# Optimization experiments

Hardware: AMD Instinct MI355X
Metric: run time of the kernel (lower is better)

Reference implementation:

```python
import jax, jax.numpy as jnp
import numpy as np

K = 10          # number of neighbors (init kwarg k)
NUM_CLASSES = 100  # label vocabulary (targets drawn in [0, 100))


def setup_inputs() -> dict:
    key = jax.random.key(0)
    k1, k2, k3 = jax.random.split(key, 3)
    X = jax.random.normal(k1, (1024, 512), dtype=jnp.float32)
    data = jax.random.normal(k2, (50000, 512), dtype=jnp.float32)
    targets = jax.random.randint(k3, (50000,), 0, NUM_CLASSES, dtype=jnp.int64)
    return {"X": X, "data": data, "targets": targets}


def reference(X, data, targets):
    # Pairwise L2 distance (p=2 path of the module), computed via the
    x2 = jnp.sum(X * X, axis=1, keepdims=True)              # [Q, 1]
    d2 = jnp.sum(data * data, axis=1)                        # [N]
    sq = x2 + d2[None, :] - 2.0 * (X @ data.T)               # [Q, N]
    dist = jnp.sqrt(jnp.maximum(sq, 0.0))                    # torch.norm(p1-p2, p=2)

    # torch: sort distances ascending, take first k indices -> top-k smallest.
    _, idx = jax.lax.top_k(-dist, K)                         # [Q, K]
    labels = targets[idx]                                    # [Q, K]

    # torch.mode over the k neighbor labels: histogram + argmax.
    # argmax picks the first (smallest) class on ties, matching torch.mode.
    counts = jax.nn.one_hot(labels, NUM_CLASSES, dtype=jnp.float32).sum(axis=1)  # [Q, C]
    pred = jnp.argmax(counts, axis=1).astype(jnp.float32)    # [Q]
    return pred
```

## Files before the change

### kernel.cpp

```cpp
#include <hip/hip_runtime.h>
#include <math.h>
#include <limits.h>

#define QN 1024
#define NN 50000
#define NPAD 50048
#define DD 512
#define KNN 10
#define NT 128
#define QTB 128
#define BK 32
#define NS 391
#define QB 8
#define NSAMP 63
#define NREST (NS - NSAMP)
#define CAP 512
#define SLACK 4.0f
#define LCAP 1152

#define WS_D2  0
#define WS_TAU 50048
#define WS_CNT (WS_TAU + 1024)
#define WS_XH  (WS_CNT + 1024)
#define WS_CKS (WS_XH + QN * DD / 2)
#define WS_BUF (WS_CKS + QN * NSAMP * KNN * 2)
#define WS_DH  (WS_BUF + QN * CAP * 2)
#define WS_END (WS_DH + NS * 16 * 2048)

typedef __attribute__((ext_vector_type(8))) short short8;
typedef __attribute__((ext_vector_type(4))) float f32x4;
typedef unsigned long long u64;

__device__ __forceinline__ u64 mkkey(float f, int idx) {
  unsigned u = __float_as_uint(f);
  unsigned m = u ^ ((unsigned)((int)u >> 31) | 0x80000000u);
  return ((u64)m << 32) | (unsigned)idx;
}

__device__ __forceinline__ float keyhi_f(unsigned m) {
  unsigned u = (m & 0x80000000u) ? (m ^ 0x80000000u) : ~m;
  return __uint_as_float(u);
}

__device__ __forceinline__ unsigned cvth(float x, float y) {
  unsigned ux = __float_as_uint(x), uy = __float_as_uint(y);
  unsigned rx = ux + 0x7fffu + ((ux >> 16) & 1u);
  unsigned ry = uy + 0x7fffu + ((uy >> 16) & 1u);
  return (rx >> 16) | (ry & 0xffff0000u);
}

__device__ __forceinline__ void glds16(const void* g, void* l) {
  __builtin_amdgcn_global_load_lds(
      (const __attribute__((address_space(1))) unsigned*)g,
      (__attribute__((address_space(3))) unsigned*)l, 16, 0, 0);
}

__device__ __forceinline__ void ins10(u64* kl, u64 k) {
#pragma unroll
  for (int u = 0; u < KNN; u++) {
    u64 lo = (k < kl[u]) ? k : kl[u];
    u64 hi = (k < kl[u]) ? kl[u] : k;
    kl[u] = lo; k = hi;
  }
}

__global__ __launch_bounds__(256) void conv_kernel(
    const float* __restrict__ dat, const float* __restrict__ Xm,
    float* __restrict__ ws) {
  if ((int)blockIdx.x >= NS) {
    const int g = ((int)blockIdx.x - NS) * 256 + threadIdx.x;
    const int b = g >> 10, kc = (g >> 6) & 15, l = g & 63;
    const int row = b * 16 + (l & 15);
    const int col = kc * 32 + (l >> 4) * 8;
    const float4* p = (const float4*)(Xm + (size_t)row * DD + col);
    float4 v0 = p[0], v1 = p[1];
    ((uint4*)(ws + WS_XH))[g] = make_uint4(
        cvth(v0.x, v0.y), cvth(v0.z, v0.w), cvth(v1.x, v1.y), cvth(v1.z, v1.w));
    return;
  }
  const int slice = blockIdx.x;
  const int t = threadIdx.x;
  const int row = t >> 1, h2 = t & 1;
  const int gr = slice * NT + row;
  const int r15 = row & 15;
  float s = 0.f;
#pragma unroll
  for (int kc8 = 0; kc8 < 8; kc8++) {
    const int kc = h2 * 8 + kc8;
    float4 v[8];
    if (gr < NN) {
      const float4* src = (const float4*)(dat + (size_t)gr * DD + kc * 32);
#pragma unroll
      for (int j = 0; j < 8; j++) v[j] = src[j];
    } else {
#pragma unroll
      for (int j = 0; j < 8; j++) v[j] = make_float4(0.f, 0.f, 0.f, 0.f);
    }
    unsigned hw[16];
#pragma unroll
    for (int j = 0; j < 8; j++) {
      s = fmaf(v[j].x, v[j].x, s); s = fmaf(v[j].y, v[j].y, s);
      s = fmaf(v[j].z, v[j].z, s); s = fmaf(v[j].w, v[j].w, s);
      hw[2 * j]     = cvth(v[j].x, v[j].y);
      hw[2 * j + 1] = cvth(v[j].z, v[j].w);
    }
    uint4* dhp = (uint4*)((unsigned char*)(ws + WS_DH) +
                          (((size_t)slice * 16 + kc) * 8 + (row >> 4)) * 1024);
#pragma unroll
    for (int qd = 0; qd < 4; qd++)
      dhp[qd * 16 + r15] = make_uint4(hw[4 * qd], hw[4 * qd + 1], hw[4 * qd + 2], hw[4 * qd + 3]);
  }
  s += __shfl_xor(s, 1, 64);
  if (h2 == 0) ws[WS_D2 + gr] = (gr < NN) ? s : __builtin_inff();
}

struct StageT { unsigned char bh[8192]; };
struct EpiT  { float sq[64][132]; };
struct ListT { u64 kl[64][4][KNN]; };

template <int MODE> struct SmemSel {
  union U { StageT s; EpiT e; ListT l; };
};
template <> struct SmemSel<1> {
  struct U { StageT s; float tau[128]; };
};

template <int PRE, int MODE>
__global__ __launch_bounds__(256, 3) void knn_chunk(
    const float* __restrict__ dat, float* __restrict__ ws, int soff) {
  __shared__ __align__(16) typename SmemSel<MODE>::U sm;
  int bqx, bsy;
  if (MODE == 1 && (gridDim.y & 7) == 0) {
    const int n = (int)(blockIdx.y * gridDim.x + blockIdx.x);
    const int m = n >> 3;
    const int ypx = (int)(gridDim.y >> 3);
    bqx = m & 7;
    bsy = (n & 7) * ypx + (m >> 3);
  } else {
    bqx = blockIdx.x; bsy = blockIdx.y;
  }
  const int qbase = bqx * QTB;
  const int slice = bsy + soff;
  const int nbase = slice * NT;
  const int t = threadIdx.x;
  const int lane = t & 63, wave = t >> 6;
  const int wn = wave & 1, wq = wave >> 1;
  const unsigned char* dh = (const unsigned char*)(ws + WS_DH);
  const char* xfh = (const char*)(ws + WS_XH);
  const int abase = (((bqx * 8 + wq * 4) * 16) * 64 + lane) * 16;

  f32x4 acc[4][4];
#pragma unroll
  for (int i = 0; i < 4; i++)
#pragma unroll
    for (int j = 0; j < 4; j++) acc[i][j] = (f32x4)0.f;

  auto stageB = [&](int kc) {
#pragma unroll
    for (int i = 0; i < 2; i++) {
      int p = wave * 2 + i;
      const unsigned char* g = dh +
          (((size_t)slice * 16 + kc) * 8 + p) * 1024 + lane * 16;
      glds16(g, sm.s.bh + p * 1024);
    }
  };

  if (PRE) {
    stageB(0);
    for (int kc = 0; kc < 16; kc++) {
      short8 fah[4];
#pragma unroll
      for (int i = 0; i < 4; i++)
        fah[i] = *(const short8*)(xfh + abase + i * 16384 + kc * 1024);
      __syncthreads();
      const int fragoff = lane * 16;
      short8 fbh[4];
#pragma unroll
      for (int i = 0; i < 4; i++)
        fbh[i] = *(const short8*)(sm.s.bh + (wn * 4 + i) * 1024 + fragoff);
      __syncthreads();
      if (kc < 15) stageB(kc + 1);
#pragma unroll
      for (int mt = 0; mt < 4; mt++)
#pragma unroll
        for (int nt = 0; nt < 4; nt++)
          acc[mt][nt] = __builtin_amdgcn_mfma_f32_16x16x32_bf16(fah[mt], fbh[nt], acc[mt][nt], 0, 0, 0);
    }
  } else {
    const int brow = t >> 1, bh_half = t & 1;
    const int bgr = nbase + brow;
    const int bpanel = (brow >> 4) * 1024;
    const int bchunk = (brow & 15) * 16;
    for (int kc = 0; kc < 16; kc++) {
      const int kk = kc * BK;
      short8 fah[4];
#pragma unroll
      for (int i = 0; i < 4; i++)
        fah[i] = *(const short8*)(xfh + abase + i * 16384 + kc * 1024);
      __syncthreads();
      {
        float4 v0 = make_float4(0.f, 0.f, 0.f, 0.f), v1 = v0, v2 = v0, v3 = v0;
        if (bgr < NN) {
          const float4* src = (const float4*)(dat + (size_t)bgr * DD + kk + bh_half * 16);
          v0 = src[0]; v1 = src[1]; v2 = src[2]; v3 = src[3];
        }
        unsigned char* bhp = sm.s.bh + bpanel;
        *(uint4*)(bhp + (2 * bh_half) * 256 + bchunk) =
            make_uint4(cvth(v0.x, v0.y), cvth(v0.z, v0.w), cvth(v1.x, v1.y), cvth(v1.z, v1.w));
        *(uint4*)(bhp + (2 * bh_half + 1) * 256 + bchunk) =
            make_uint4(cvth(v2.x, v2.y), cvth(v2.z, v2.w), cvth(v3.x, v3.y), cvth(v3.z, v3.w));
      }
      __syncthreads();
      const int fragoff = lane * 16;
      short8 fbh[4];
#pragma unroll
      for (int i = 0; i < 4; i++)
        fbh[i] = *(const short8*)(sm.s.bh + (wn * 4 + i) * 1024 + fragoff);
      __syncthreads();
#pragma unroll
      for (int mt = 0; mt < 4; mt++)
#pragma unroll
        for (int nt = 0; nt < 4; nt++)
          acc[mt][nt] = __builtin_amdgcn_mfma_f32_16x16x32_bf16(fah[mt], fbh[nt], acc[mt][nt], 0, 0, 0);
    }
  }

  if constexpr (MODE == 0) {
#pragma unroll
    for (int pass = 0; pass < 2; pass++) {
      __syncthreads();
      if (wq == pass) {
#pragma unroll
        for (int nt = 0; nt < 4; nt++) {
          int col = wn * 64 + nt * 16 + (lane & 15);
          float d2v = ws[WS_D2 + nbase + col];
#pragma unroll
          for (int mt = 0; mt < 4; mt++)
#pragma unroll
            for (int rg = 0; rg < 4; rg++) {
              int lr = mt * 16 + (lane >> 4) * 4 + rg;
              sm.e.sq[lr][col] = fmaf(-2.f, acc[mt][nt][rg], d2v);
            }
        }
      }
      __syncthreads();
      {
        const int r = t >> 2, s = t & 3;
        u64 kl[KNN];
#pragma unroll
        for (int u = 0; u < KNN; u++) kl[u] = ~0ull;
        for (int jj = 0; jj < 32; jj++) {
          int c = s * 32 + ((jj + r + 8 * s) & 31);
          float v = sm.e.sq[r][c];
          ins10(kl, mkkey(v, nbase + c));
        }
        __syncthreads();
#pragma unroll
        for (int u = 0; u < KNN; u++) sm.l.kl[r][s][u] = kl[u];
      }
      __syncthreads();
      if (t < 64) {
        u64* dst = ((u64*)(ws + WS_CKS)) +
                   ((size_t)(qbase + pass * 64 + t) * NSAMP + blockIdx.y) * KNN;
        int h0 = 0, h1 = 0, h2 = 0, h3 = 0;
        for (int pick = 0; pick < KNN; pick++) {
          u64 k0 = sm.l.kl[t][0][h0], k1 = sm.l.kl[t][1][h1];
          u64 k2 = sm.l.kl[t][2][h2], k3 = sm.l.kl[t][3][h3];
          u64 best = k0; int bm = 0;
          if (k1 < best) { best = k1; bm = 1; }
          if (k2 < best) { best = k2; bm = 2; }
          if (k3 < best) { best = k3; bm = 3; }
          dst[pick] = best;
          h0 += (bm == 0); h1 += (bm == 1); h2 += (bm == 2); h3 += (bm == 3);
        }
      }
    }
  } else {
    if (t < 128) sm.tau[t] = ws[WS_TAU + qbase + t];
    __syncthreads();
    unsigned* cnt = (unsigned*)(ws + WS_CNT);
    u64* buf = (u64*)(ws + WS_BUF);
    float d2v[4];
#pragma unroll
    for (int nt = 0; nt < 4; nt++)
      d2v[nt] = ws[WS_D2 + nbase + wn * 64 + nt * 16 + (lane & 15)];
#pragma unroll
    for (int mt = 0; mt < 4; mt++)
#pragma unroll
      for (int rg = 0; rg < 4; rg++) {
        int row = wq * 64 + mt * 16 + (lane >> 4) * 4 + rg;
        float tr = sm.tau[row];
#pragma unroll
        for (int nt = 0; nt < 4; nt++) {
          float d = fmaf(-2.f, acc[mt][nt][rg], d2v[nt]);
          if (d < tr) {
            int col = nbase + wn * 64 + nt * 16 + (lane & 15);
            int q = qbase + row;
            unsigned slot = atomicAdd(cnt + q, 1u);
            if (slot < CAP) buf[(size_t)q * CAP + slot] = mkkey(d, col);
          }
        }
      }
  }
}

__global__ __launch_bounds__(64) void tau_kernel(float* __restrict__ ws) {
  const int q = blockIdx.x;
  const int t = threadIdx.x;
  const u64* samp = ((const u64*)(ws + WS_CKS)) + (size_t)q * NSAMP * KNN;
  const int NC = NSAMP * KNN;
  u64 kl[KNN];
#pragma unroll
  for (int u = 0; u < KNN; u++) kl[u] = ~0ull;
  for (int j = t; j < NC; j += 64) ins10(kl, samp[j]);
  __shared__ u64 wk[64][KNN];
  __shared__ u64 m2[8][KNN];
#pragma unroll
  for (int u = 0; u < KNN; u++) wk[t][u] = kl[u];
  __syncthreads();
  if (t < 8) {
    int h[8] = {0, 0, 0, 0, 0, 0, 0, 0};
    for (int pick = 0; pick < KNN; pick++) {
      u64 best = ~0ull; int bm = 0;
#pragma unroll
      for (int m = 0; m < 8; m++) {
        u64 km = wk[t * 8 + m][h[m]];
        if (km < best) { best = km; bm = m; }
      }
      m2[t][pick] = best;
#pragma unroll
      for (int m = 0; m < 8; m++) h[m] += (bm == m);
    }
  }
  __syncthreads();
  if (t == 0) {
    int h[8] = {0, 0, 0, 0, 0, 0, 0, 0};
    u64 best = 0;
    for (int pick = 0; pick < KNN; pick++) {
      best = ~0ull; int bm = 0;
#pragma unroll
      for (int m = 0; m < 8; m++) {
        u64 km = m2[m][h[m]];
        if (km < best) { best = km; bm = m; }
      }
#pragma unroll
      for (int m = 0; m < 8; m++) h[m] += (bm == m);
    }
    ws[WS_TAU + q] = keyhi_f((unsigned)(best >> 32)) + SLACK;
    ((unsigned*)(ws + WS_CNT))[q] = 0u;
  }
}

__global__ __launch_bounds__(256) void knn_final(
    const int* __restrict__ targets, const float* __restrict__ Xm,
    const float* __restrict__ dat, float* __restrict__ ws,
    float* __restrict__ out) {
  const int q = blockIdx.x;
  const int t = threadIdx.x;
  const int lane = t & 63, wave = t >> 6;
  __shared__ float qrow[DD];
  __shared__ unsigned lst[LCAP];
  __shared__ int nlist;
  __shared__ u64 wk4[4][KNN];
  if (t == 0) nlist = 0;
  if (t < 128) ((float4*)qrow)[t] = ((const float4*)(Xm + (size_t)q * DD))[t];
  __syncthreads();
  const float tr = ws[WS_TAU + q];
  const u64* samp = ((const u64*)(ws + WS_CKS)) + (size_t)q * NSAMP * KNN;
  for (int j = t; j < NSAMP * KNN; j += 256) {
    u64 k = samp[j];
    if (keyhi_f((unsigned)(k >> 32)) < tr) {
      int s_ = atomicAdd(&nlist, 1);
      if (s_ < LCAP) lst[s_] = (unsigned)k;
    }
  }
  unsigned c = ((const unsigned*)(ws + WS_CNT))[q];
  if (c > CAP) c = CAP;
  const u64* buf = ((const u64*)(ws + WS_BUF)) + (size_t)q * CAP;
  for (int j = t; j < (int)c; j += 256) {
    int s_ = atomicAdd(&nlist, 1);
    if (s_ < LCAP) lst[s_] = (unsigned)buf[j];
  }
  __syncthreads();
  const int n = nlist < LCAP ? nlist : LCAP;

  u64 kl[KNN];
#pragma unroll
  for (int u = 0; u < KNN; u++) kl[u] = ~0ull;
  const float4* qv = (const float4*)qrow;
  const float4 q0 = qv[lane * 2], q1 = qv[lane * 2 + 1];
  for (int j = wave; j < n; j += 4) {
    const unsigned idx = lst[j];
    const float4* xr = (const float4*)(dat + (size_t)idx * DD) + lane * 2;
    const float4 a0 = xr[0], a1 = xr[1];
    float p = a0.x * q0.x;
    p = fmaf(a0.y, q0.y, p); p = fmaf(a0.z, q0.z, p); p = fmaf(a0.w, q0.w, p);
    p = fmaf(a1.x, q1.x, p); p = fmaf(a1.y, q1.y, p);
    p = fmaf(a1.z, q1.z, p); p = fmaf(a1.w, q1.w, p);
#pragma unroll
    for (int s_ = 1; s_ < 64; s_ <<= 1) p += __shfl_xor(p, s_, 64);
    float d = fmaf(-2.f, p, ws[WS_D2 + idx]);
    ins10(kl, mkkey(d, (int)idx));
  }
  if (lane == 0)
#pragma unroll
    for (int u = 0; u < KNN; u++) wk4[wave][u] = kl[u];
  __syncthreads();
  if (t == 0) {
    int h[4] = {0, 0, 0, 0};
    int fi[KNN];
    for (int pick = 0; pick < KNN; pick++) {
      u64 best = ~0ull; int bm = 0;
#pragma unroll
      for (int m = 0; m < 4; m++) {
        u64 km = wk4[m][h[m]];
        if (km < best) { best = km; bm = m; }
      }
      fi[pick] = (int)(unsigned)(best & 0xffffffffu);
      h[bm]++;
    }
    int lab[KNN];
#pragma unroll
    for (int u = 0; u < KNN; u++) lab[u] = targets[fi[u]];
    int bc = 0, bl = INT_MAX;
#pragma unroll
    for (int i = 0; i < KNN; i++) {
      int cc = 0;
#pragma unroll
      for (int j = 0; j < KNN; j++) cc += (lab[j] == lab[i]) ? 1 : 0;
      if (cc > bc || (cc == bc && lab[i] < bl)) { bc = cc; bl = lab[i]; }
    }
    out[q] = (float)bl;
  }
}

extern "C" void kernel_launch(void* const* d_in, const int* in_sizes, int n_in,
                              void* d_out, int out_size, void* d_ws, size_t ws_size,
                              hipStream_t stream) {
  const float* Xm  = (const float*)d_in[0];
  const float* dat = (const float*)d_in[1];
  const int* targets = (const int*)d_in[2];
  float* out = (float*)d_out;
  float* ws  = (float*)d_ws;
  const bool pre = ws_size >= (size_t)WS_END * 4;

  hipLaunchKernelGGL(conv_kernel, dim3(NS + QN * DD / 8 / 256), dim3(256), 0,
                     stream, dat, Xm, ws);
  if (pre) {
    hipLaunchKernelGGL((knn_chunk<1, 0>), dim3(QB, NSAMP), dim3(256), 0, stream, dat, ws, 0);
    hipLaunchKernelGGL(tau_kernel, dim3(QN), dim3(64), 0, stream, ws);
    hipLaunchKernelGGL((knn_chunk<1, 1>), dim3(QB, NREST), dim3(256), 0, stream, dat, ws, NSAMP);
  } else {
    hipLaunchKernelGGL((knn_chunk<0, 0>), dim3(QB, NSAMP), dim3(256), 0, stream, dat, ws, 0);
    hipLaunchKernelGGL(tau_kernel, dim3(QN), dim3(64), 0, stream, ws);
    hipLaunchKernelGGL((knn_chunk<0, 1>), dim3(QB, NREST), dim3(256), 0, stream, dat, ws, NSAMP);
  }
  hipLaunchKernelGGL(knn_final, dim3(QN), dim3(256), 0, stream, targets, Xm, dat, ws, out);
}
```

Baseline: 317.5 us.

## Halve sample slices, register-prefetch GEMM fragments, and unroll the exact rerank loop

Reduces the number of sampled slices used to estimate the per-query threshold from 63 to 31, shrinking the first-pass work. The precomputed-B GEMM path drops the global-to-LDS staging and its barriers, loading A and B fragments straight into registers with one-step software prefetch. The exact rerank loop processes two candidates per wave iteration and skips the insertion when a key cannot enter the top-10. A looser threshold from fewer samples may admit more candidates and overflow the buffer caps, and the register-only path raises register pressure and loses LDS sharing of B across waves.

```diff
diff --git a/kernel.cpp b/kernel.cpp
--- a/kernel.cpp
+++ b/kernel.cpp
@@ -12,7 +12,7 @@
 #define BK 32
 #define NS 391
 #define QB 8
-#define NSAMP 63
+#define NSAMP 31
 #define NREST (NS - NSAMP)
 #define CAP 512
 #define SLACK 4.0f
@@ -47,12 +47,6 @@
   unsigned rx = ux + 0x7fffu + ((ux >> 16) & 1u);
   unsigned ry = uy + 0x7fffu + ((uy >> 16) & 1u);
   return (rx >> 16) | (ry & 0xffff0000u);
-}
-
-__device__ __forceinline__ void glds16(const void* g, void* l) {
-  __builtin_amdgcn_global_load_lds(
-      (const __attribute__((address_space(1))) unsigned*)g,
-      (__attribute__((address_space(3))) unsigned*)l, 16, 0, 0);
 }
 
 __device__ __forceinline__ void ins10(u64* kl, u64 k) {
@@ -118,17 +112,16 @@
 struct EpiT  { float sq[64][132]; };
 struct ListT { u64 kl[64][4][KNN]; };
 
-template <int MODE> struct SmemSel {
-  union U { StageT s; EpiT e; ListT l; };
-};
-template <> struct SmemSel<1> {
-  struct U { StageT s; float tau[128]; };
-};
+template <int PRE, int MODE> struct Smem;
+template <> struct Smem<1, 0> { union { EpiT e; ListT l; }; };
+template <> struct Smem<1, 1> { float tau[128]; };
+template <> struct Smem<0, 0> { union { StageT s; EpiT e; ListT l; }; };
+template <> struct Smem<0, 1> { StageT s; float tau[128]; };
 
 template <int PRE, int MODE>
 __global__ __launch_bounds__(256, 3) void knn_chunk(
     const float* __restrict__ dat, float* __restrict__ ws, int soff) {
-  __shared__ __align__(16) typename SmemSel<MODE>::U sm;
+  __shared__ __align__(16) Smem<PRE, MODE> sm;
   int bqx, bsy;
   if (MODE == 1 && (gridDim.y & 7) == 0) {
     const int n = (int)(blockIdx.y * gridDim.x + blockIdx.x);
@@ -148,6 +141,7 @@
   const unsigned char* dh = (const unsigned char*)(ws + WS_DH);
   const char* xfh = (const char*)(ws + WS_XH);
   const int abase = (((bqx * 8 + wq * 4) * 16) * 64 + lane) * 16;
+  const unsigned char* bbase = dh + ((size_t)slice * 16 * 8 + wn * 4) * 1024 + lane * 16;
 
   f32x4 acc[4][4];
 #pragma unroll
@@ -155,36 +149,32 @@
 #pragma unroll
     for (int j = 0; j < 4; j++) acc[i][j] = (f32x4)0.f;
 
-  auto stageB = [&](int kc) {
-#pragma unroll
-    for (int i = 0; i < 2; i++) {
-      int p = wave * 2 + i;
-      const unsigned char* g = dh +
-          (((size_t)slice * 16 + kc) * 8 + p) * 1024 + lane * 16;
-      glds16(g, sm.s.bh + p * 1024);
-    }
-  };
-
-  if (PRE) {
-    stageB(0);
+  if constexpr (PRE == 1) {
+    short8 ca[4], cb[4];
+#pragma unroll
+    for (int i = 0; i < 4; i++) {
+      ca[i] = *(const short8*)(xfh + abase + i * 16384);
+      cb[i] = *(const short8*)(bbase + i * 1024);
+    }
+#pragma unroll
     for (int kc = 0; kc < 16; kc++) {
-      short8 fah[4];
-#pragma unroll
-      for (int i = 0; i < 4; i++)
-        fah[i] = *(const short8*)(xfh + abase + i * 16384 + kc * 1024);
-      __syncthreads();
-      const int fragoff = lane * 16;
-      short8 fbh[4];
-#pragma unroll
-      for (int i = 0; i < 4; i++)
-        fbh[i] = *(const short8*)(sm.s.bh + (wn * 4 + i) * 1024 + fragoff);
-      __syncthreads();
-      if (kc < 15) stageB(kc + 1);
+      short8 na[4], nb[4];
+      if (kc < 15) {
+#pragma unroll
+        for (int i = 0; i < 4; i++) {
+          na[i] = *(const short8*)(xfh + abase + i * 16384 + (kc + 1) * 1024);
+          nb[i] = *(const short8*)(bbase + ((kc + 1) * 8 + i) * 1024);
+        }
+      }
 #pragma unroll
       for (int mt = 0; mt < 4; mt++)
 #pragma unroll
         for (int nt = 0; nt < 4; nt++)
-          acc[mt][nt] = __builtin_amdgcn_mfma_f32_16x16x32_bf16(fah[mt], fbh[nt], acc[mt][nt], 0, 0, 0);
+          acc[mt][nt] = __builtin_amdgcn_mfma_f32_16x16x32_bf16(ca[mt], cb[nt], acc[mt][nt], 0, 0, 0);
+      if (kc < 15) {
+#pragma unroll
+        for (int i = 0; i < 4; i++) { ca[i] = na[i]; cb[i] = nb[i]; }
+      }
     }
   } else {
     const int brow = t >> 1, bh_half = t & 1;
@@ -389,18 +379,35 @@
   for (int u = 0; u < KNN; u++) kl[u] = ~0ull;
   const float4* qv = (const float4*)qrow;
   const float4 q0 = qv[lane * 2], q1 = qv[lane * 2 + 1];
-  for (int j = wave; j < n; j += 4) {
-    const unsigned idx = lst[j];
-    const float4* xr = (const float4*)(dat + (size_t)idx * DD) + lane * 2;
-    const float4 a0 = xr[0], a1 = xr[1];
-    float p = a0.x * q0.x;
-    p = fmaf(a0.y, q0.y, p); p = fmaf(a0.z, q0.z, p); p = fmaf(a0.w, q0.w, p);
-    p = fmaf(a1.x, q1.x, p); p = fmaf(a1.y, q1.y, p);
-    p = fmaf(a1.z, q1.z, p); p = fmaf(a1.w, q1.w, p);
-#pragma unroll
-    for (int s_ = 1; s_ < 64; s_ <<= 1) p += __shfl_xor(p, s_, 64);
-    float d = fmaf(-2.f, p, ws[WS_D2 + idx]);
-    ins10(kl, mkkey(d, (int)idx));
+  for (int j = wave; j < n; j += 8) {
+    const unsigned i0 = lst[j];
+    const int has1 = (j + 4) < n;
+    const unsigned i1 = has1 ? lst[j + 4] : i0;
+    const float4* x0 = (const float4*)(dat + (size_t)i0 * DD) + lane * 2;
+    const float4* x1 = (const float4*)(dat + (size_t)i1 * DD) + lane * 2;
+    const float4 a0 = x0[0], a1 = x0[1];
+    const float4 b0 = x1[0], b1 = x1[1];
+    float p0 = a0.x * q0.x, p1 = b0.x * q0.x;
+    p0 = fmaf(a0.y, q0.y, p0); p1 = fmaf(b0.y, q0.y, p1);
+    p0 = fmaf(a0.z, q0.z, p0); p1 = fmaf(b0.z, q0.z, p1);
+    p0 = fmaf(a0.w, q0.w, p0); p1 = fmaf(b0.w, q0.w, p1);
+    p0 = fmaf(a1.x, q1.x, p0); p1 = fmaf(b1.x, q1.x, p1);
+    p0 = fmaf(a1.y, q1.y, p0); p1 = fmaf(b1.y, q1.y, p1);
+    p0 = fmaf(a1.z, q1.z, p0); p1 = fmaf(b1.z, q1.z, p1);
+    p0 = fmaf(a1.w, q1.w, p0); p1 = fmaf(b1.w, q1.w, p1);
+#pragma unroll
+    for (int s_ = 1; s_ < 64; s_ <<= 1) {
+      p0 += __shfl_xor(p0, s_, 64);
+      p1 += __shfl_xor(p1, s_, 64);
+    }
+    float d0 = fmaf(-2.f, p0, ws[WS_D2 + i0]);
+    u64 k0 = mkkey(d0, (int)i0);
+    if (k0 < kl[KNN - 1]) ins10(kl, k0);
+    if (has1) {
+      float d1 = fmaf(-2.f, p1, ws[WS_D2 + i1]);
+      u64 k1 = mkkey(d1, (int)i1);
+      if (k1 < kl[KNN - 1]) ins10(kl, k1);
+    }
   }
   if (lane == 0)
 #pragma unroll
```

After: 367.5 us. 1.16x slower.
